# Optimization experiments

Hardware: AMD Instinct MI355X
Metric: run time of the kernel (lower is better)

The kernel has to match this reference:

```python
import jax, jax.numpy as jnp
import numpy as np

TAU = 0.07        # temperature from init_kwargs
EPS = 1e-8        # torch F.cosine_similarity eps
NEG_INF = -1e9    # mask fill value used by the original module


def setup_inputs() -> dict:
    key = jax.random.key(0)
    k1, k2 = jax.random.split(key)
    B, D = 4096, 512
    anchor = jax.random.normal(k1, (B, D), dtype=jnp.float32)
    positive = jax.random.normal(k2, (B, D), dtype=jnp.float32)
    return {"anchor": anchor, "positive": positive}


def reference(anchor, positive):
    B = anchor.shape[0]
    N = 2 * B
    emb = jnp.concatenate([anchor, positive], axis=0)          # (2B, D)
    # cosine similarity matrix == normalized dot products (same math as the
    # broadcasted F.cosine_similarity, without the O(N^2 D) intermediate)
    norm = jnp.maximum(jnp.linalg.norm(emb, axis=1, keepdims=True), EPS)
    z = emb / norm
    sim = jnp.matmul(z, z.T) / TAU                             # (2B, 2B)

    idx = jnp.arange(N)
    pos_idx = (idx + B) % N                                    # positive pair index
    pos_logits = sim[idx, pos_idx][:, None]                    # (2B, 1)

    # negatives: everything except self and the positive pair
    neg_mask = (
        jnp.ones((N, N), dtype=bool)
        .at[idx, idx].set(False)
        .at[idx, pos_idx].set(False)
    )
    neg_logits = jnp.where(neg_mask, sim, NEG_INF)             # (2B, 2B)

    all_logits = jnp.concatenate([pos_logits, neg_logits], axis=1)  # (2B, 2B+1)
    loss_per_sample = -pos_logits[:, 0] + jax.scipy.special.logsumexp(all_logits, axis=1)
    # every row has a positive, so valid_samples is all-True; reduction='mean'
    return loss_per_sample.mean()
```

## Files before the change

kernel.cpp:

```cpp
#include <hip/hip_runtime.h>
#include <hip/hip_bf16.h>
#include <stdint.h>


#define N_TOT   8192
#define B_HALF  4096
#define DDIM    512
#define INV_TAU 14.285714285714286f

typedef __bf16 bf16x8 __attribute__((ext_vector_type(8)));
typedef __bf16 bf16x4 __attribute__((ext_vector_type(4)));
typedef float  floatx4 __attribute__((ext_vector_type(4)));

__device__ __forceinline__ void gl2lds16(const void* g, void* l) {
    __builtin_amdgcn_global_load_lds(
        (const __attribute__((address_space(1))) void*)g,
        (__attribute__((address_space(3))) void*)l, 16, 0, 0);
}

__global__ __launch_bounds__(256) void knorm(const float* __restrict__ anchor,
                                             const float* __restrict__ positive,
                                             __bf16* __restrict__ z,
                                             float* __restrict__ row_sums,
                                             float* __restrict__ out) {
    const int row  = blockIdx.x * 4 + (threadIdx.x >> 6);
    const int lane = threadIdx.x & 63;
    if (lane == 0) row_sums[row] = 0.0f;
    if (blockIdx.x == 0 && threadIdx.x == 0) out[0] = 0.0f;
    const float* src = (row < B_HALF) ? (anchor + (size_t)row * DDIM)
                                      : (positive + (size_t)(row - B_HALF) * DDIM);
    float4 v0 = ((const float4*)src)[lane];
    float4 v1 = ((const float4*)src)[lane + 64];
    float ss = v0.x*v0.x + v0.y*v0.y + v0.z*v0.z + v0.w*v0.w
             + v1.x*v1.x + v1.y*v1.y + v1.z*v1.z + v1.w*v1.w;
    #pragma unroll
    for (int m = 1; m < 64; m <<= 1) ss += __shfl_xor(ss, m, 64);
    const float inv = 1.0f / fmaxf(sqrtf(ss), 1e-8f);
    bf16x4 o0, o1;
    o0[0] = (__bf16)(v0.x*inv); o0[1] = (__bf16)(v0.y*inv);
    o0[2] = (__bf16)(v0.z*inv); o0[3] = (__bf16)(v0.w*inv);
    o1[0] = (__bf16)(v1.x*inv); o1[1] = (__bf16)(v1.y*inv);
    o1[2] = (__bf16)(v1.z*inv); o1[3] = (__bf16)(v1.w*inv);
    bf16x4* dst = (bf16x4*)(z + (size_t)row * DDIM);
    dst[lane]      = o0;
    dst[lane + 64] = o1;
}

__global__ __launch_bounds__(256, 4) void ksim(const __bf16* __restrict__ z,
                                               float* __restrict__ row_sums,
                                               float* __restrict__ pos_sims) {
    const int bid = (int)blockIdx.x;
    int rem = (bid & 7) * 260 + (bid >> 3);
    int gr = 0, gc = 0;
    for (;;) {
        const int sz = (gr == gc) ? 36 : 64;
        if (rem < sz) break;
        rem -= sz;
        if (++gc == 8) { gr++; gc = gr; }
    }
    int rt, ct;
    if (gr == gc) {
        int i = 0;
        while (rem >= 8 - i) { rem -= 8 - i; i++; }
        rt = gr * 8 + i;
        ct = gc * 8 + i + rem;
    } else {
        rt = gr * 8 + (rem >> 3);
        ct = gc * 8 + (rem & 7);
    }
    const bool diag = (rt == ct);
    const bool posb = (ct == rt + 32);

    const int r0 = rt * 128, c0 = ct * 128;
    const int tid  = threadIdx.x;
    const int w    = tid >> 6, lane = tid & 63;
    const int quad = lane >> 4, nlo = lane & 15;
    const int wrow = (w >> 1) * 64, wcol = (w & 1) * 64;

    __shared__ __align__(16) char smem[32768];
    char* As = smem;
    char* Bs = smem + 16384;
    const char* Bbase = diag ? As : Bs;

    floatx4 acc[4][4];
    #pragma unroll
    for (int a = 0; a < 4; a++)
        #pragma unroll
        for (int b = 0; b < 4; b++) acc[a][b] = (floatx4){0.f, 0.f, 0.f, 0.f};

    const int srow = lane >> 3;
    const int p    = lane & 7;

    for (int kb = 0; kb < DDIM; kb += 64) {
        #pragma unroll
        for (int it = 0; it < 4; it++) {
            const int c  = w * 4 + it;
            const int rr = c * 8 + srow;
            const int lc = (p - rr) & 7;
            gl2lds16(z + (size_t)(r0 + rr) * DDIM + kb + lc * 8, As + c * 1024);
            if (!diag)
                gl2lds16(z + (size_t)(c0 + rr) * DDIM + kb + lc * 8, Bs + c * 1024);
        }
        __syncthreads();

        #pragma unroll
        for (int ks = 0; ks < 2; ks++) {
            bf16x8 af[4], bfr[4];
            #pragma unroll
            for (int mi = 0; mi < 4; mi++) {
                const int rr = wrow + mi * 16 + nlo;
                const int pc = (ks * 4 + quad + rr) & 7;
                af[mi] = *(const bf16x8*)(As + rr * 128 + pc * 16);
            }
            #pragma unroll
            for (int ni = 0; ni < 4; ni++) {
                const int rr = wcol + ni * 16 + nlo;
                const int pc = (ks * 4 + quad + rr) & 7;
                bfr[ni] = *(const bf16x8*)(Bbase + rr * 128 + pc * 16);
            }
            #pragma unroll
            for (int mi = 0; mi < 4; mi++)
                #pragma unroll
                for (int ni = 0; ni < 4; ni++)
                    acc[mi][ni] = __builtin_amdgcn_mfma_f32_16x16x32_bf16(
                        af[mi], bfr[ni], acc[mi][ni], 0, 0, 0);
        }
        __syncthreads();
    }

    if (diag) {
        #pragma unroll
        for (int mi = 0; mi < 4; mi++) {
            #pragma unroll
            for (int reg = 0; reg < 4; reg++) {
                const int i = r0 + wrow + mi * 16 + quad * 4 + reg;
                float rs = 0.f;
                #pragma unroll
                for (int ni = 0; ni < 4; ni++) {
                    const int j2 = c0 + wcol + ni * 16 + nlo;
                    const float e = __expf(acc[mi][ni][reg] * INV_TAU - INV_TAU);
                    rs += (j2 == i) ? 0.f : e;
                }
                rs += __shfl_xor(rs, 1, 64);
                rs += __shfl_xor(rs, 2, 64);
                rs += __shfl_xor(rs, 4, 64);
                rs += __shfl_xor(rs, 8, 64);
                if (nlo == 0) atomicAdd(&row_sums[i], rs);
            }
        }
    } else {
        float cs[4] = {0.f, 0.f, 0.f, 0.f};
        #pragma unroll
        for (int mi = 0; mi < 4; mi++) {
            #pragma unroll
            for (int reg = 0; reg < 4; reg++) {
                const int i = r0 + wrow + mi * 16 + quad * 4 + reg;
                const int ipos = i ^ B_HALF;
                float rs = 0.f;
                #pragma unroll
                for (int ni = 0; ni < 4; ni++) {
                    const int j2 = c0 + wcol + ni * 16 + nlo;
                    const float sim = acc[mi][ni][reg] * INV_TAU;
                    const float e = __expf(sim - INV_TAU);
                    if (posb && j2 == ipos) {
                        pos_sims[i]  = sim;
                        pos_sims[j2] = sim;
                    }
                    rs += e;
                    cs[ni] += e;
                }
                rs += __shfl_xor(rs, 1, 64);
                rs += __shfl_xor(rs, 2, 64);
                rs += __shfl_xor(rs, 4, 64);
                rs += __shfl_xor(rs, 8, 64);
                if (nlo == 0) atomicAdd(&row_sums[i], rs);
            }
        }
        #pragma unroll
        for (int ni = 0; ni < 4; ni++) {
            float c = cs[ni];
            c += __shfl_xor(c, 16, 64);
            c += __shfl_xor(c, 32, 64);
            if (quad == 0)
                atomicAdd(&row_sums[c0 + wcol + ni * 16 + nlo], c);
        }
    }
}

__global__ __launch_bounds__(256) void kfinal(const float* __restrict__ row_sums,
                                              const float* __restrict__ pos_sims,
                                              float* __restrict__ out) {
    const int r = blockIdx.x * 256 + threadIdx.x;
    float v = INV_TAU + __logf(row_sums[r]) - pos_sims[r];
    #pragma unroll
    for (int m = 1; m < 64; m <<= 1) v += __shfl_xor(v, m, 64);
    __shared__ float wsum[4];
    if ((threadIdx.x & 63) == 0) wsum[threadIdx.x >> 6] = v;
    __syncthreads();
    if (threadIdx.x == 0)
        atomicAdd(out, (wsum[0] + wsum[1] + wsum[2] + wsum[3]) * (1.0f / (float)N_TOT));
}

extern "C" void kernel_launch(void* const* d_in, const int* in_sizes, int n_in,
                              void* d_out, int out_size, void* d_ws, size_t ws_size,
                              hipStream_t stream) {
    const float* anchor   = (const float*)d_in[0];
    const float* positive = (const float*)d_in[1];
    float* out = (float*)d_out;

    char* ws = (char*)d_ws;
    __bf16* z        = (__bf16*)ws;
    float*  row_sums = (float*)(ws + 8388608);
    float*  pos_sims = (float*)(ws + 8388608 + 32768);

    knorm<<<N_TOT / 4, 256, 0, stream>>>(anchor, positive, z, row_sums, out);
    ksim<<<2080, 256, 0, stream>>>(z, row_sums, pos_sims);
    kfinal<<<N_TOT / 256, 256, 0, stream>>>(row_sums, pos_sims, out);
}
```

Measured before the change: 129.9 us.

## Quantize normalized embeddings to FP8 and compute positive logits exactly in fp32

The normalized embeddings are now stored as FP8 instead of bf16, and the similarity GEMM uses the fp8 MFMA with a K-step of 128 bytes per tile load. This halves the bytes loaded and doubles MFMA throughput per instruction. To keep the positive-pair logit accurate, the norm kernel computes the anchor/positive dot product in fp32 and writes pos_sims directly. The GEMM excludes that entry from the row sums, and the final kernel adds it back exactly. The cost is reduced precision for the negative logits.

Result: faster. 111.0 us, median of 3 (-14.5%).

```diff
diff --git a/kernel.cpp b/kernel.cpp
--- a/kernel.cpp
+++ b/kernel.cpp
@@ -8,9 +8,7 @@
 #define DDIM    512
 #define INV_TAU 14.285714285714286f
 
-typedef __bf16 bf16x8 __attribute__((ext_vector_type(8)));
-typedef __bf16 bf16x4 __attribute__((ext_vector_type(4)));
-typedef float  floatx4 __attribute__((ext_vector_type(4)));
+typedef float floatx4 __attribute__((ext_vector_type(4)));
 
 __device__ __forceinline__ void gl2lds16(const void* g, void* l) {
     __builtin_amdgcn_global_load_lds(
@@ -20,35 +18,59 @@
 
 __global__ __launch_bounds__(256) void knorm(const float* __restrict__ anchor,
                                              const float* __restrict__ positive,
-                                             __bf16* __restrict__ z,
+                                             uint8_t* __restrict__ z,
                                              float* __restrict__ row_sums,
+                                             float* __restrict__ pos_sims,
                                              float* __restrict__ out) {
-    const int row  = blockIdx.x * 4 + (threadIdx.x >> 6);
+    const int w    = threadIdx.x >> 6;
     const int lane = threadIdx.x & 63;
-    if (lane == 0) row_sums[row] = 0.0f;
+    const int row  = blockIdx.x * 4 + w;
+    const int prow = row + B_HALF;
     if (blockIdx.x == 0 && threadIdx.x == 0) out[0] = 0.0f;
-    const float* src = (row < B_HALF) ? (anchor + (size_t)row * DDIM)
-                                      : (positive + (size_t)(row - B_HALF) * DDIM);
-    float4 v0 = ((const float4*)src)[lane];
-    float4 v1 = ((const float4*)src)[lane + 64];
-    float ss = v0.x*v0.x + v0.y*v0.y + v0.z*v0.z + v0.w*v0.w
-             + v1.x*v1.x + v1.y*v1.y + v1.z*v1.z + v1.w*v1.w;
+
+    const float* a = anchor   + (size_t)row * DDIM;
+    const float* p = positive + (size_t)row * DDIM;
+    float4 a0 = ((const float4*)a)[lane];
+    float4 a1 = ((const float4*)a)[lane + 64];
+    float4 p0 = ((const float4*)p)[lane];
+    float4 p1 = ((const float4*)p)[lane + 64];
+
+    float ssa = a0.x*a0.x + a0.y*a0.y + a0.z*a0.z + a0.w*a0.w
+              + a1.x*a1.x + a1.y*a1.y + a1.z*a1.z + a1.w*a1.w;
+    float ssp = p0.x*p0.x + p0.y*p0.y + p0.z*p0.z + p0.w*p0.w
+              + p1.x*p1.x + p1.y*p1.y + p1.z*p1.z + p1.w*p1.w;
+    float dot = a0.x*p0.x + a0.y*p0.y + a0.z*p0.z + a0.w*p0.w
+              + a1.x*p1.x + a1.y*p1.y + a1.z*p1.z + a1.w*p1.w;
     #pragma unroll
-    for (int m = 1; m < 64; m <<= 1) ss += __shfl_xor(ss, m, 64);
-    const float inv = 1.0f / fmaxf(sqrtf(ss), 1e-8f);
-    bf16x4 o0, o1;
-    o0[0] = (__bf16)(v0.x*inv); o0[1] = (__bf16)(v0.y*inv);
-    o0[2] = (__bf16)(v0.z*inv); o0[3] = (__bf16)(v0.w*inv);
-    o1[0] = (__bf16)(v1.x*inv); o1[1] = (__bf16)(v1.y*inv);
-    o1[2] = (__bf16)(v1.z*inv); o1[3] = (__bf16)(v1.w*inv);
-    bf16x4* dst = (bf16x4*)(z + (size_t)row * DDIM);
-    dst[lane]      = o0;
-    dst[lane + 64] = o1;
-}
-
-__global__ __launch_bounds__(256, 4) void ksim(const __bf16* __restrict__ z,
-                                               float* __restrict__ row_sums,
-                                               float* __restrict__ pos_sims) {
+    for (int m = 1; m < 64; m <<= 1) {
+        ssa += __shfl_xor(ssa, m, 64);
+        ssp += __shfl_xor(ssp, m, 64);
+        dot += __shfl_xor(dot, m, 64);
+    }
+    const float inva = 1.0f / fmaxf(sqrtf(ssa), 1e-8f);
+    const float invp = 1.0f / fmaxf(sqrtf(ssp), 1e-8f);
+    const float psim = dot * inva * invp * INV_TAU;
+    if (lane == 0) {
+        pos_sims[row]  = psim;  pos_sims[prow] = psim;
+        row_sums[row]  = 0.0f;  row_sums[prow] = 0.0f;
+    }
+
+    uint32_t qa0 = __builtin_amdgcn_cvt_pk_fp8_f32(a0.x*inva, a0.y*inva, 0, 0);
+    qa0          = __builtin_amdgcn_cvt_pk_fp8_f32(a0.z*inva, a0.w*inva, qa0, 1);
+    uint32_t qa1 = __builtin_amdgcn_cvt_pk_fp8_f32(a1.x*inva, a1.y*inva, 0, 0);
+    qa1          = __builtin_amdgcn_cvt_pk_fp8_f32(a1.z*inva, a1.w*inva, qa1, 1);
+    uint32_t qp0 = __builtin_amdgcn_cvt_pk_fp8_f32(p0.x*invp, p0.y*invp, 0, 0);
+    qp0          = __builtin_amdgcn_cvt_pk_fp8_f32(p0.z*invp, p0.w*invp, qp0, 1);
+    uint32_t qp1 = __builtin_amdgcn_cvt_pk_fp8_f32(p1.x*invp, p1.y*invp, 0, 0);
+    qp1          = __builtin_amdgcn_cvt_pk_fp8_f32(p1.z*invp, p1.w*invp, qp1, 1);
+    uint32_t* za = (uint32_t*)(z + (size_t)row  * DDIM);
+    uint32_t* zp = (uint32_t*)(z + (size_t)prow * DDIM);
+    za[lane] = qa0; za[lane + 64] = qa1;
+    zp[lane] = qp0; zp[lane + 64] = qp1;
+}
+
+__global__ __launch_bounds__(256, 4) void ksim(const uint8_t* __restrict__ z,
+                                               float* __restrict__ row_sums) {
     const int bid = (int)blockIdx.x;
     int rem = (bid & 7) * 260 + (bid >> 3);
     int gr = 0, gc = 0;
@@ -91,38 +113,42 @@
     const int srow = lane >> 3;
     const int p    = lane & 7;
 
-    for (int kb = 0; kb < DDIM; kb += 64) {
+    for (int kb = 0; kb < 4; kb++) {
         #pragma unroll
         for (int it = 0; it < 4; it++) {
             const int c  = w * 4 + it;
             const int rr = c * 8 + srow;
             const int lc = (p - rr) & 7;
-            gl2lds16(z + (size_t)(r0 + rr) * DDIM + kb + lc * 8, As + c * 1024);
+            gl2lds16(z + (size_t)(r0 + rr) * DDIM + kb * 128 + lc * 16,
+                     As + c * 1024);
             if (!diag)
-                gl2lds16(z + (size_t)(c0 + rr) * DDIM + kb + lc * 8, Bs + c * 1024);
+                gl2lds16(z + (size_t)(c0 + rr) * DDIM + kb * 128 + lc * 16,
+                         Bs + c * 1024);
         }
         __syncthreads();
 
         #pragma unroll
-        for (int ks = 0; ks < 2; ks++) {
-            bf16x8 af[4], bfr[4];
+        for (int ks = 0; ks < 4; ks++) {
+            const int g  = ks * 4 + quad;
+            const int lc = g >> 1, h = g & 1;
+            long af[4], bfr[4];
             #pragma unroll
             for (int mi = 0; mi < 4; mi++) {
                 const int rr = wrow + mi * 16 + nlo;
-                const int pc = (ks * 4 + quad + rr) & 7;
-                af[mi] = *(const bf16x8*)(As + rr * 128 + pc * 16);
+                const int pc = (lc + rr) & 7;
+                af[mi] = *(const long*)(As + rr * 128 + pc * 16 + h * 8);
             }
             #pragma unroll
             for (int ni = 0; ni < 4; ni++) {
                 const int rr = wcol + ni * 16 + nlo;
-                const int pc = (ks * 4 + quad + rr) & 7;
-                bfr[ni] = *(const bf16x8*)(Bbase + rr * 128 + pc * 16);
+                const int pc = (lc + rr) & 7;
+                bfr[ni] = *(const long*)(Bbase + rr * 128 + pc * 16 + h * 8);
             }
             #pragma unroll
             for (int mi = 0; mi < 4; mi++)
                 #pragma unroll
                 for (int ni = 0; ni < 4; ni++)
-                    acc[mi][ni] = __builtin_amdgcn_mfma_f32_16x16x32_bf16(
+                    acc[mi][ni] = __builtin_amdgcn_mfma_f32_16x16x32_fp8_fp8(
                         af[mi], bfr[ni], acc[mi][ni], 0, 0, 0);
         }
         __syncthreads();
@@ -160,12 +186,8 @@
                 #pragma unroll
                 for (int ni = 0; ni < 4; ni++) {
                     const int j2 = c0 + wcol + ni * 16 + nlo;
-                    const float sim = acc[mi][ni][reg] * INV_TAU;
-                    const float e = __expf(sim - INV_TAU);
-                    if (posb && j2 == ipos) {
-                        pos_sims[i]  = sim;
-                        pos_sims[j2] = sim;
-                    }
+                    float e = __expf(acc[mi][ni][reg] * INV_TAU - INV_TAU);
+                    if (posb && j2 == ipos) e = 0.f;
                     rs += e;
                     cs[ni] += e;
                 }
@@ -191,7 +213,8 @@
                                               const float* __restrict__ pos_sims,
                                               float* __restrict__ out) {
     const int r = blockIdx.x * 256 + threadIdx.x;
-    float v = INV_TAU + __logf(row_sums[r]) - pos_sims[r];
+    const float ps = pos_sims[r];
+    float v = INV_TAU + __logf(row_sums[r] + __expf(ps - INV_TAU)) - ps;
     #pragma unroll
     for (int m = 1; m < 64; m <<= 1) v += __shfl_xor(v, m, 64);
     __shared__ float wsum[4];
@@ -209,11 +232,12 @@
     float* out = (float*)d_out;
 
     char* ws = (char*)d_ws;
-    __bf16* z        = (__bf16*)ws;
-    float*  row_sums = (float*)(ws + 8388608);
-    float*  pos_sims = (float*)(ws + 8388608 + 32768);
-
-    knorm<<<N_TOT / 4, 256, 0, stream>>>(anchor, positive, z, row_sums, out);
-    ksim<<<2080, 256, 0, stream>>>(z, row_sums, pos_sims);
+    uint8_t* z        = (uint8_t*)ws;
+    float*   row_sums = (float*)(ws + 4194304);
+    float*   pos_sims = (float*)(ws + 4194304 + 32768);
+
+    knorm<<<B_HALF / 4, 256, 0, stream>>>(anchor, positive, z, row_sums,
+                                          pos_sims, out);
+    ksim<<<2080, 256, 0, stream>>>(z, row_sums);
     kfinal<<<N_TOT / 256, 256, 0, stream>>>(row_sums, pos_sims, out);
 }
```
